# Kernel tuning notes

Hardware: AMD Instinct MI355X
Metric: run time of the kernel (lower is better)

## Reference

```python
import jax, jax.numpy as jnp
import numpy as np

B, M, K = 8, 4096, 16
C = 64       # input_dim
D = 64       # d_model


def _lin(key, fan_in, fan_out):
    k1, k2 = jax.random.split(key)
    bound = 1.0 / np.sqrt(fan_in)
    W = jax.random.uniform(k1, (fan_out, fan_in), minval=-bound, maxval=bound, dtype=jnp.float32)
    b = jax.random.uniform(k2, (fan_out,), minval=-bound, maxval=bound, dtype=jnp.float32)
    return W, b


def setup_inputs() -> dict:
    key = jax.random.key(0)
    ks = jax.random.split(key, 12)
    x = jax.random.normal(ks[0], (B, M, K, C), dtype=jnp.float32)
    xyz = jax.random.normal(ks[1], (B, M, K, 3), dtype=jnp.float32)
    Wq, bq = _lin(ks[2], C, D)
    Wk, bk = _lin(ks[3], C, D)
    Wv, bv = _lin(ks[4], C, D)
    Wp1, bp1 = _lin(ks[5], 3, D)
    Wp2, bp2 = _lin(ks[6], D, D)
    Wa1, ba1 = _lin(ks[7], D, D)
    Wa2, ba2 = _lin(ks[8], D, D)
    W2, b2 = _lin(ks[9], D, C)
    return dict(x=x, xyz=xyz, Wq=Wq, bq=bq, Wk=Wk, bk=bk, Wv=Wv, bv=bv,
                Wp1=Wp1, bp1=bp1, Wp2=Wp2, bp2=bp2,
                Wa1=Wa1, ba1=ba1, Wa2=Wa2, ba2=ba2, W2=W2, b2=b2)


def reference(x, xyz, Wq, bq, Wk, bk, Wv, bv, Wp1, bp1, Wp2, bp2,
              Wa1, ba1, Wa2, ba2, W2, b2):
    lin = lambda t, W, b: jnp.matmul(t, W.T) + b
    raw_feature = x[:, :, 0, :]                 # [B,M,C]
    raw_xyz = xyz[:, :, 0:1, :]                 # [B,M,1,3]
    q = lin(raw_feature, Wq, bq)                # [B,M,D]
    k = lin(x, Wk, bk)                          # [B,M,K,D]
    v = lin(x, Wv, bv)                          # [B,M,K,D]
    rel = xyz - raw_xyz                         # [B,M,K,3]
    pos_enc = lin(jax.nn.relu(lin(rel, Wp1, bp1)), Wp2, bp2)  # [B,M,K,D]
    h = q[:, :, None, :] - k + pos_enc          # [B,M,K,D]
    attn_logits = lin(jax.nn.relu(lin(h, Wa1, ba1)), Wa2, ba2)
    attn = jax.nn.softmax(attn_logits / np.sqrt(D), axis=-2)  # softmax over K
    res = jnp.einsum('bmnf,bmnf->bmf', attn, v + pos_enc)
    return lin(res, W2, b2) + raw_feature       # [B,M,C]
```

## Files before the change

kernel.cpp:

```cpp
#include <hip/hip_runtime.h>

#define NM 4096
#define NK 16
#define NC 64

typedef __attribute__((ext_vector_type(8))) short s8v;
typedef __attribute__((ext_vector_type(4))) float f4v;
typedef __attribute__((ext_vector_type(2))) unsigned int u2v;

__device__ __forceinline__ short f2bf(float f) {
  return __builtin_bit_cast(short, (__bf16)f);
}
__device__ __forceinline__ float bf2f(unsigned short s) {
  return __builtin_bit_cast(float, ((unsigned)s) << 16);
}
__device__ __forceinline__ s8v pack8(f4v a, f4v b) {
  s8v r;
  r[0]=f2bf(a[0]); r[1]=f2bf(a[1]); r[2]=f2bf(a[2]); r[3]=f2bf(a[3]);
  r[4]=f2bf(b[0]); r[5]=f2bf(b[1]); r[6]=f2bf(b[2]); r[7]=f2bf(b[3]);
  return r;
}

#define MFMA(a,b,c) __builtin_amdgcn_mfma_f32_16x16x32_bf16((a),(b),(c),0,0,0)

#define HSTRIDE 72
#define TB16 (16*HSTRIDE)

__global__ void precomp_kernel(const float* __restrict__ Wq, const float* __restrict__ bq,
                               const float* __restrict__ Wk, const float* __restrict__ bk,
                               const float* __restrict__ Wp2,const float* __restrict__ bp2,
                               const float* __restrict__ Wa1,const float* __restrict__ ba1,
                               float* __restrict__ ws) {
  const int gid = blockIdx.x * 256 + threadIdx.x;
  if (gid < 3*4096) {
    const int m = gid >> 12, e = gid & 4095, i = e >> 6, j = e & 63;
    const float* R = Wa1 + i*64;
    float s = 0.f;
    if (m == 0)      { for (int l = 0; l < 64; ++l) s += R[l] * Wq [l*64 + j]; }
    else if (m == 1) { for (int l = 0; l < 64; ++l) s -= R[l] * Wk [l*64 + j]; }
    else             { for (int l = 0; l < 64; ++l) s += R[l] * Wp2[l*64 + j]; }
    ws[gid] = s;
  } else if (gid < 3*4096 + 64) {
    const int i = gid - 3*4096;
    const float* R = Wa1 + i*64;
    float s = 0.f;
    for (int l = 0; l < 64; ++l) s += R[l] * bq[l];
    ws[gid] = s;
  } else if (gid < 3*4096 + 128) {
    const int i = gid - (3*4096 + 64);
    const float* R = Wa1 + i*64;
    float s = ba1[i];
    for (int l = 0; l < 64; ++l) s += R[l] * (bp2[l] - bk[l]);
    ws[gid] = s;
  }
}

__global__ void precomp2_kernel(const float* __restrict__ Wv,
                                const float* __restrict__ Wp2,
                                const float* __restrict__ Wa2,
                                const float* __restrict__ W2,
                                float* __restrict__ ws) {
  const int g = blockIdx.x * 256 + threadIdx.x;
  if (g >= 7*512) return;
  const int mat = g >> 9, rem = g & 511;
  const int f = rem >> 6, ln = rem & 63;
  const int t = f >> 1, h = f & 1;
  const int cc = ln & 15, qq = ln >> 4;
  const int n = 16*t + cc;
  const float* W =
    (mat==0) ? ws + 4096 :
    (mat==1) ? Wv :
    (mat==2) ? Wp2 :
    (mat==3) ? ws + 8192 :
    (mat==4) ? Wa2 :
    (mat==5) ? ws :
               W2;
  short* dst = (short*)(ws + 12544) + (size_t)g * 8;
  s8v v;
  #pragma unroll
  for (int j = 0; j < 8; ++j) {
    const int kp = h*32 + qq*8 + j;
    int k;
    if (mat == 4)                  k = 16*(2*h + (j>>2)) + 4*qq + (j&3);
    else if (mat == 2 || mat == 3) k = ((kp & 3) << 4) | (kp >> 2);
    else                           k = kp;
    v[j] = f2bf(W[n*64 + k]);
  }
  *(s8v*)dst = v;
}

__global__ __attribute__((amdgpu_flat_work_group_size(256, 256)))
           __attribute__((amdgpu_waves_per_eu(1, 8)))
void lattn_kernel(const float* __restrict__ x,  const float* __restrict__ xyz,
                  const float* __restrict__ Wp1,const float* __restrict__ bp1,
                  const float* __restrict__ Wp2,const float* __restrict__ bp2,
                  const float* __restrict__ Wv, const float* __restrict__ bv,
                  const float* __restrict__ Wa2,const float* __restrict__ ba2,
                  const float* __restrict__ W2, const float* __restrict__ b2,
                  const float* __restrict__ ws,
                  float* __restrict__ out) {
  __shared__ __align__(16) short wlds[5*8*64*8];
  __shared__ __align__(16) short qres[4*TB16];
  __shared__ __align__(16) f4v  wp1t[4*17];
  __shared__ float bvpet[64];
  __shared__ float ba2t[64];

  const int tid = threadIdx.x;
  const float* bqa = ws + 12288;
  const float* bcv = ws + 12352;
  const short* wsb = (const short*)(ws + 12544);

  #pragma unroll
  for (int i = 0; i < 10; ++i) {
    const int g = tid + i*256;
    *(s8v*)&wlds[(size_t)g*8] = *(const s8v*)&wsb[(size_t)g*8];
  }
  if (tid < 64) {
    const int lqv = tid >> 4, ii = tid & 15;
    const int jj = ii & 7, h = ii >> 3;
    const int n = 16*(jj&3) + 2*lqv + (jj>>2) + 8*h;
    f4v t4;
    t4[0] = Wp1[n*3+0]; t4[1] = Wp1[n*3+1]; t4[2] = Wp1[n*3+2]; t4[3] = bp1[n];
    wp1t[lqv*17 + ii] = t4;
  } else if (tid < 128) {
    const int n = tid - 64;
    bvpet[n] = bv[n] + bp2[n];
  } else if (tid < 192) {
    const int n = tid - 128;
    ba2t[n] = ba2[n];
  }
  __syncthreads();

  const int w    = tid >> 6;
  const int lane = tid & 63;
  const int c    = lane & 15;
  const int lq   = lane >> 4;

  const int gw  = blockIdx.x * 4 + w;
  const int gp0 = gw << 4;
  const int b   = gp0 >> 12;
  const int m0  = gp0 & (NM - 1);

  short* qbuf = qres + w * TB16;

  const long ptbase = (long)(b * NM + m0);

  {
    const float* xr = x + (ptbase + c) * (long)(NK*NC) + 8*lq;
    s8v rA0 = pack8(*(const f4v*)xr,        *(const f4v*)(xr+4));
    s8v rA1 = pack8(*(const f4v*)(xr+32),   *(const f4v*)(xr+36));
    #pragma unroll
    for (int t = 0; t < 4; ++t) {
      s8v w0 = *(const s8v*)&wsb[(size_t)(5*512 + 2*t*64 + lane)*8];
      s8v w1 = *(const s8v*)&wsb[(size_t)(5*512 + (2*t+1)*64 + lane)*8];
      const float bb = bqa[16*t + c];
      f4v acc = {bb, bb, bb, bb};
      acc = MFMA(rA0, w0, acc);
      acc = MFMA(rA1, w1, acc);
      const float bcf = bcv[16*t + c];
      #pragma unroll
      for (int r = 0; r < 4; ++r)
        qbuf[(4*lq + r)*HSTRIDE + 16*t + c] = f2bf(acc[r] + bcf);
    }
  }

  f4v na0, na1, na2, na3, nb0, nb1, nb2, nb3;
  float nzaa[3], nzba[3], nzab[3], nzbb[3];
  {
    const float* xra = x + ptbase * (long)(NK*NC) + c*NC + 8*lq;
    na0 = *(const f4v*)xra;      na1 = *(const f4v*)(xra+4);
    na2 = *(const f4v*)(xra+32); na3 = *(const f4v*)(xra+36);
    const float* xrb = xra + NK*NC;
    nb0 = *(const f4v*)xrb;      nb1 = *(const f4v*)(xrb+4);
    nb2 = *(const f4v*)(xrb+32); nb3 = *(const f4v*)(xrb+36);
    const float* zpa = xyz + ptbase * (long)(NK*3);
    nzaa[0]=zpa[c*3+0]; nzaa[1]=zpa[c*3+1]; nzaa[2]=zpa[c*3+2];
    nzba[0]=zpa[0];     nzba[1]=zpa[1];     nzba[2]=zpa[2];
    const float* zpb = zpa + NK*3;
    nzab[0]=zpb[c*3+0]; nzab[1]=zpb[c*3+1]; nzab[2]=zpb[c*3+2];
    nzbb[0]=zpb[0];     nzbb[1]=zpb[1];     nzbb[2]=zpb[2];
  }

  #pragma unroll 1
  for (int pp = 0; pp < 16; pp += 2) {
    s8v xAa0 = pack8(na0, na1), xAa1 = pack8(na2, na3);
    s8v xAb0 = pack8(nb0, nb1), xAb1 = pack8(nb2, nb3);
    const float rxa = nzaa[0]-nzba[0], rya = nzaa[1]-nzba[1], rza = nzaa[2]-nzba[2];
    const float rxb = nzab[0]-nzbb[0], ryb = nzab[1]-nzbb[1], rzb = nzab[2]-nzbb[2];
    if (pp < 14) {
      const long prow = ptbase + pp + 2;
      const float* xra = x + prow * (long)(NK*NC) + c*NC + 8*lq;
      na0 = *(const f4v*)xra;      na1 = *(const f4v*)(xra+4);
      na2 = *(const f4v*)(xra+32); na3 = *(const f4v*)(xra+36);
      const float* xrb = xra + NK*NC;
      nb0 = *(const f4v*)xrb;      nb1 = *(const f4v*)(xrb+4);
      nb2 = *(const f4v*)(xrb+32); nb3 = *(const f4v*)(xrb+36);
      const float* zpa = xyz + prow * (long)(NK*3);
      nzaa[0]=zpa[c*3+0]; nzaa[1]=zpa[c*3+1]; nzaa[2]=zpa[c*3+2];
      nzba[0]=zpa[0];     nzba[1]=zpa[1];     nzba[2]=zpa[2];
      const float* zpb = zpa + NK*3;
      nzab[0]=zpb[c*3+0]; nzab[1]=zpb[c*3+1]; nzab[2]=zpb[c*3+2];
      nzbb[0]=zpb[0];     nzbb[1]=zpb[1];     nzbb[2]=zpb[2];
    }

    s8v pAa0, pAa1, pAb0, pAb1;
    #pragma unroll
    for (int i = 0; i < 8; ++i) {
      f4v w0v = wp1t[lq*17 + i];
      f4v w1v = wp1t[lq*17 + 8 + i];
      float a0 = fmaxf(fmaf(w0v[0], rxa, fmaf(w0v[1], rya, fmaf(w0v[2], rza, w0v[3]))), 0.0f);
      float a1 = fmaxf(fmaf(w1v[0], rxa, fmaf(w1v[1], rya, fmaf(w1v[2], rza, w1v[3]))), 0.0f);
      float b0 = fmaxf(fmaf(w0v[0], rxb, fmaf(w0v[1], ryb, fmaf(w0v[2], rzb, w0v[3]))), 0.0f);
      float b1 = fmaxf(fmaf(w1v[0], rxb, fmaf(w1v[1], ryb, fmaf(w1v[2], rzb, w1v[3]))), 0.0f);
      pAa0[i] = f2bf(a0); pAa1[i] = f2bf(a1);
      pAb0[i] = f2bf(b0); pAb1[i] = f2bf(b1);
    }

    f4v sa[4], sb[4];
    #pragma unroll
    for (int t = 0; t < 4; ++t) {
      u2v qa2 = *(const u2v*)&qbuf[pp*HSTRIDE + 16*t + 4*lq];
      u2v qb2 = *(const u2v*)&qbuf[(pp+1)*HSTRIDE + 16*t + 4*lq];
      f4v acca, accb;
      acca[0] = __builtin_bit_cast(float, qa2[0] << 16);
      acca[1] = __builtin_bit_cast(float, qa2[0] & 0xffff0000u);
      acca[2] = __builtin_bit_cast(float, qa2[1] << 16);
      acca[3] = __builtin_bit_cast(float, qa2[1] & 0xffff0000u);
      accb[0] = __builtin_bit_cast(float, qb2[0] << 16);
      accb[1] = __builtin_bit_cast(float, qb2[0] & 0xffff0000u);
      accb[2] = __builtin_bit_cast(float, qb2[1] << 16);
      accb[3] = __builtin_bit_cast(float, qb2[1] & 0xffff0000u);
      const short* wb = &wlds[(0*512 + 2*t*64 + lane) * 8];
      s8v w0 = *(const s8v*)wb;
      s8v w1 = *(const s8v*)(wb + 512);
      acca = MFMA(w0, xAa0, acca);  acca = MFMA(w1, xAa1, acca);
      accb = MFMA(w0, xAb0, accb);  accb = MFMA(w1, xAb1, accb);
      sa[t] = acca; sb[t] = accb;
    }
    #pragma unroll
    for (int t = 0; t < 4; ++t) {
      const short* wb = &wlds[(3*512 + 2*t*64 + lane) * 8];
      s8v w0 = *(const s8v*)wb;
      s8v w1 = *(const s8v*)(wb + 512);
      f4v acca = MFMA(w0, pAa0, sa[t]);  acca = MFMA(w1, pAa1, acca);
      f4v accb = MFMA(w0, pAb0, sb[t]);  accb = MFMA(w1, pAb1, accb);
      #pragma unroll
      for (int r = 0; r < 4; ++r) {
        sa[t][r] = fmaxf(acca[r], 0.0f);
        sb[t][r] = fmaxf(accb[r], 0.0f);
      }
    }
    s8v aAa0 = pack8(sa[0], sa[1]), aAa1 = pack8(sa[2], sa[3]);
    s8v aAb0 = pack8(sb[0], sb[1]), aAb1 = pack8(sb[2], sb[3]);

    #pragma unroll
    for (int t = 0; t < 4; ++t) {
      const short* wb4 = &wlds[(4*512 + 2*t*64 + lane) * 8];
      s8v w40 = *(const s8v*)wb4;
      s8v w41 = *(const s8v*)(wb4 + 512);
      const float bb2 = ba2t[16*t + c];
      f4v lga = {bb2, bb2, bb2, bb2};
      f4v lgb = lga;
      lga = MFMA(aAa0, w40, lga);  lga = MFMA(aAa1, w41, lga);
      lgb = MFMA(aAb0, w40, lgb);  lgb = MFMA(aAb1, w41, lgb);

      const short* wb1 = &wlds[(1*512 + 2*t*64 + lane) * 8];
      const short* wb2 = &wlds[(2*512 + 2*t*64 + lane) * 8];
      s8v w10 = *(const s8v*)wb1;
      s8v w11 = *(const s8v*)(wb1 + 512);
      s8v w20 = *(const s8v*)wb2;
      s8v w21 = *(const s8v*)(wb2 + 512);
      const float bbv = bvpet[16*t + c];
      f4v vpa = {bbv, bbv, bbv, bbv};
      f4v vpb = vpa;
      vpa = MFMA(xAa0, w10, vpa);  vpa = MFMA(xAa1, w11, vpa);
      vpa = MFMA(pAa0, w20, vpa);  vpa = MFMA(pAa1, w21, vpa);
      vpb = MFMA(xAb0, w10, vpb);  vpb = MFMA(xAb1, w11, vpb);
      vpb = MFMA(pAb0, w20, vpb);  vpb = MFMA(pAb1, w21, vpb);

      f4v ea, eb;
      #pragma unroll
      for (int r = 0; r < 4; ++r) {
        ea[r] = exp2f(lga[r] * 0.18033688011112043f);
        eb[r] = exp2f(lgb[r] * 0.18033688011112043f);
      }
      float sma = (ea[0] + ea[1]) + (ea[2] + ea[3]);
      float smb = (eb[0] + eb[1]) + (eb[2] + eb[3]);
      sma += __shfl_xor(sma, 16);
      smb += __shfl_xor(smb, 16);
      sma += __shfl_xor(sma, 32);
      smb += __shfl_xor(smb, 32);
      float pra = 0.0f, prb = 0.0f;
      #pragma unroll
      for (int r = 0; r < 4; ++r) {
        pra += ea[r] * vpa[r];
        prb += eb[r] * vpb[r];
      }
      pra += __shfl_xor(pra, 16);
      prb += __shfl_xor(prb, 16);
      pra += __shfl_xor(pra, 32);
      prb += __shfl_xor(prb, 32);
      pra *= 1.0f / sma;
      prb *= 1.0f / smb;
      if (lq == 0) {
        qbuf[pp*HSTRIDE + 16*t + c]     = f2bf(pra);
        qbuf[(pp+1)*HSTRIDE + 16*t + c] = f2bf(prb);
      }
    }
  }

  {
    s8v resA0 = *(const s8v*)&qbuf[c*HSTRIDE + 8*lq];
    s8v resA1 = *(const s8v*)&qbuf[c*HSTRIDE + 32 + 8*lq];
    #pragma unroll
    for (int t = 0; t < 4; ++t) {
      s8v w0 = *(const s8v*)&wsb[(size_t)(6*512 + 2*t*64 + lane)*8];
      s8v w1 = *(const s8v*)&wsb[(size_t)(6*512 + (2*t+1)*64 + lane)*8];
      const float bb = b2[16*t + c];
      f4v acc = {bb, bb, bb, bb};
      acc = MFMA(resA0, w0, acc);
      acc = MFMA(resA1, w1, acc);
      #pragma unroll
      for (int r = 0; r < 4; ++r) {
        const long pr2 = ptbase + 4*lq + r;
        out[pr2*NC + 16*t + c] = acc[r] + x[pr2*(long)(NK*NC) + 16*t + c];
      }
    }
  }
}

extern "C" void kernel_launch(void* const* d_in, const int* in_sizes, int n_in,
                              void* d_out, int out_size, void* d_ws, size_t ws_size,
                              hipStream_t stream) {
  (void)in_sizes; (void)n_in; (void)out_size; (void)ws_size;
  const float* x   = (const float*)d_in[0];
  const float* xyz = (const float*)d_in[1];
  const float* Wq  = (const float*)d_in[2];
  const float* bq  = (const float*)d_in[3];
  const float* Wk  = (const float*)d_in[4];
  const float* bk  = (const float*)d_in[5];
  const float* Wv  = (const float*)d_in[6];
  const float* bv  = (const float*)d_in[7];
  const float* Wp1 = (const float*)d_in[8];
  const float* bp1 = (const float*)d_in[9];
  const float* Wp2 = (const float*)d_in[10];
  const float* bp2 = (const float*)d_in[11];
  const float* Wa1 = (const float*)d_in[12];
  const float* ba1 = (const float*)d_in[13];
  const float* Wa2 = (const float*)d_in[14];
  const float* ba2 = (const float*)d_in[15];
  const float* W2  = (const float*)d_in[16];
  const float* b2  = (const float*)d_in[17];
  float* out = (float*)d_out;
  float* ws  = (float*)d_ws;

  precomp_kernel<<<dim3(49), dim3(256), 0, stream>>>(Wq, bq, Wk, bk, Wp2, bp2, Wa1, ba1, ws);
  precomp2_kernel<<<dim3(14), dim3(256), 0, stream>>>(Wv, Wp2, Wa2, W2, ws);
  lattn_kernel<<<dim3(512), dim3(256), 0, stream>>>(
      x, xyz, Wp1, bp1, Wp2, bp2, Wv, bv, Wa2, ba2, W2, b2, ws, out);
}
```

Measured before the change: 244.5 us.

## Merge weight precompute kernels, hoist qbuf loads, add MFMA priority and fast math

Folds the two weight-preprocessing kernels into a single launch that computes the Wa1-composed products directly into the packed bf16 MFMA layout, removing one launch and the fp32 intermediate round trip. In the main kernel, the qbuf LDS reads are hoisted ahead of the position-MLP computation, s_setprio raises wave priority around the MFMA blocks, and exp2f and the reciprocal are swapped for the hardware intrinsics. Risks: each thread in the merged precompute now does redundant 64-length dot products serially, lowering its parallelism, and the fast exp and reciprocal are slightly less accurate.

```diff
diff --git a/kernel.cpp b/kernel.cpp
--- a/kernel.cpp
+++ b/kernel.cpp
@@ -10,9 +10,6 @@
 
 __device__ __forceinline__ short f2bf(float f) {
   return __builtin_bit_cast(short, (__bf16)f);
-}
-__device__ __forceinline__ float bf2f(unsigned short s) {
-  return __builtin_bit_cast(float, ((unsigned)s) << 16);
 }
 __device__ __forceinline__ s8v pack8(f4v a, f4v b) {
   s8v r;
@@ -30,63 +27,59 @@
                                const float* __restrict__ Wk, const float* __restrict__ bk,
                                const float* __restrict__ Wp2,const float* __restrict__ bp2,
                                const float* __restrict__ Wa1,const float* __restrict__ ba1,
+                               const float* __restrict__ Wv, const float* __restrict__ Wa2,
+                               const float* __restrict__ W2,
                                float* __restrict__ ws) {
   const int gid = blockIdx.x * 256 + threadIdx.x;
-  if (gid < 3*4096) {
-    const int m = gid >> 12, e = gid & 4095, i = e >> 6, j = e & 63;
-    const float* R = Wa1 + i*64;
-    float s = 0.f;
-    if (m == 0)      { for (int l = 0; l < 64; ++l) s += R[l] * Wq [l*64 + j]; }
-    else if (m == 1) { for (int l = 0; l < 64; ++l) s -= R[l] * Wk [l*64 + j]; }
-    else             { for (int l = 0; l < 64; ++l) s += R[l] * Wp2[l*64 + j]; }
-    ws[gid] = s;
-  } else if (gid < 3*4096 + 64) {
-    const int i = gid - 3*4096;
+  if (gid < 7*512) {
+    const int g = gid;
+    const int mat = g >> 9, rem = g & 511;
+    const int f = rem >> 6, ln = rem & 63;
+    const int t = f >> 1, h = f & 1;
+    const int cc = ln & 15, qq = ln >> 4;
+    const int n = 16*t + cc;
+    short* dst = (short*)(ws + 12544) + (size_t)g * 8;
+    s8v v;
+    #pragma unroll
+    for (int j = 0; j < 8; ++j) {
+      const int kp = h*32 + qq*8 + j;
+      int k;
+      if (mat == 4)                  k = 16*(2*h + (j>>2)) + 4*qq + (j&3);
+      else if (mat == 2 || mat == 3) k = ((kp & 3) << 4) | (kp >> 2);
+      else                           k = kp;
+      float val;
+      if (mat == 0) {
+        const float* R = Wa1 + n*64; float s = 0.f;
+        for (int l = 0; l < 64; ++l) s -= R[l] * Wk[l*64 + k];
+        val = s;
+      } else if (mat == 3) {
+        const float* R = Wa1 + n*64; float s = 0.f;
+        for (int l = 0; l < 64; ++l) s += R[l] * Wp2[l*64 + k];
+        val = s;
+      } else if (mat == 5) {
+        const float* R = Wa1 + n*64; float s = 0.f;
+        for (int l = 0; l < 64; ++l) s += R[l] * Wq[l*64 + k];
+        val = s;
+      } else {
+        const float* W = (mat==1) ? Wv : (mat==2) ? Wp2 : (mat==4) ? Wa2 : W2;
+        val = W[n*64 + k];
+      }
+      v[j] = f2bf(val);
+    }
+    *(s8v*)dst = v;
+  } else if (gid < 7*512 + 64) {
+    const int i = gid - 7*512;
     const float* R = Wa1 + i*64;
     float s = 0.f;
     for (int l = 0; l < 64; ++l) s += R[l] * bq[l];
-    ws[gid] = s;
-  } else if (gid < 3*4096 + 128) {
-    const int i = gid - (3*4096 + 64);
+    ws[12288 + i] = s;
+  } else if (gid < 7*512 + 128) {
+    const int i = gid - (7*512 + 64);
     const float* R = Wa1 + i*64;
     float s = ba1[i];
     for (int l = 0; l < 64; ++l) s += R[l] * (bp2[l] - bk[l]);
-    ws[gid] = s;
-  }
-}
-
-__global__ void precomp2_kernel(const float* __restrict__ Wv,
-                                const float* __restrict__ Wp2,
-                                const float* __restrict__ Wa2,
-                                const float* __restrict__ W2,
-                                float* __restrict__ ws) {
-  const int g = blockIdx.x * 256 + threadIdx.x;
-  if (g >= 7*512) return;
-  const int mat = g >> 9, rem = g & 511;
-  const int f = rem >> 6, ln = rem & 63;
-  const int t = f >> 1, h = f & 1;
-  const int cc = ln & 15, qq = ln >> 4;
-  const int n = 16*t + cc;
-  const float* W =
-    (mat==0) ? ws + 4096 :
-    (mat==1) ? Wv :
-    (mat==2) ? Wp2 :
-    (mat==3) ? ws + 8192 :
-    (mat==4) ? Wa2 :
-    (mat==5) ? ws :
-               W2;
-  short* dst = (short*)(ws + 12544) + (size_t)g * 8;
-  s8v v;
-  #pragma unroll
-  for (int j = 0; j < 8; ++j) {
-    const int kp = h*32 + qq*8 + j;
-    int k;
-    if (mat == 4)                  k = 16*(2*h + (j>>2)) + 4*qq + (j&3);
-    else if (mat == 2 || mat == 3) k = ((kp & 3) << 4) | (kp >> 2);
-    else                           k = kp;
-    v[j] = f2bf(W[n*64 + k]);
-  }
-  *(s8v*)dst = v;
+    ws[12352 + i] = s;
+  }
 }
 
 __global__ __attribute__((amdgpu_flat_work_group_size(256, 256)))
@@ -203,6 +196,15 @@
       nzbb[0]=zpb[0];     nzbb[1]=zpb[1];     nzbb[2]=zpb[2];
     }
 
+    u2v qa2_0 = *(const u2v*)&qbuf[pp*HSTRIDE +  0 + 4*lq];
+    u2v qa2_1 = *(const u2v*)&qbuf[pp*HSTRIDE + 16 + 4*lq];
+    u2v qa2_2 = *(const u2v*)&qbuf[pp*HSTRIDE + 32 + 4*lq];
+    u2v qa2_3 = *(const u2v*)&qbuf[pp*HSTRIDE + 48 + 4*lq];
+    u2v qb2_0 = *(const u2v*)&qbuf[(pp+1)*HSTRIDE +  0 + 4*lq];
+    u2v qb2_1 = *(const u2v*)&qbuf[(pp+1)*HSTRIDE + 16 + 4*lq];
+    u2v qb2_2 = *(const u2v*)&qbuf[(pp+1)*HSTRIDE + 32 + 4*lq];
+    u2v qb2_3 = *(const u2v*)&qbuf[(pp+1)*HSTRIDE + 48 + 4*lq];
+
     s8v pAa0, pAa1, pAb0, pAb1;
     #pragma unroll
     for (int i = 0; i < 8; ++i) {
@@ -217,10 +219,11 @@
     }
 
     f4v sa[4], sb[4];
-    #pragma unroll
-    for (int t = 0; t < 4; ++t) {
-      u2v qa2 = *(const u2v*)&qbuf[pp*HSTRIDE + 16*t + 4*lq];
-      u2v qb2 = *(const u2v*)&qbuf[(pp+1)*HSTRIDE + 16*t + 4*lq];
+    __builtin_amdgcn_s_setprio(1);
+    #pragma unroll
+    for (int t = 0; t < 4; ++t) {
+      u2v qa2 = (t==0) ? qa2_0 : (t==1) ? qa2_1 : (t==2) ? qa2_2 : qa2_3;
+      u2v qb2 = (t==0) ? qb2_0 : (t==1) ? qb2_1 : (t==2) ? qb2_2 : qb2_3;
       f4v acca, accb;
       acca[0] = __builtin_bit_cast(float, qa2[0] << 16);
       acca[1] = __builtin_bit_cast(float, qa2[0] & 0xffff0000u);
@@ -250,6 +253,7 @@
         sb[t][r] = fmaxf(accb[r], 0.0f);
       }
     }
+    __builtin_amdgcn_s_setprio(0);
     s8v aAa0 = pack8(sa[0], sa[1]), aAa1 = pack8(sa[2], sa[3]);
     s8v aAb0 = pack8(sb[0], sb[1]), aAb1 = pack8(sb[2], sb[3]);
 
@@ -259,6 +263,7 @@
       s8v w40 = *(const s8v*)wb4;
       s8v w41 = *(const s8v*)(wb4 + 512);
       const float bb2 = ba2t[16*t + c];
+      __builtin_amdgcn_s_setprio(1);
       f4v lga = {bb2, bb2, bb2, bb2};
       f4v lgb = lga;
       lga = MFMA(aAa0, w40, lga);  lga = MFMA(aAa1, w41, lga);
@@ -277,12 +282,13 @@
       vpa = MFMA(pAa0, w20, vpa);  vpa = MFMA(pAa1, w21, vpa);
       vpb = MFMA(xAb0, w10, vpb);  vpb = MFMA(xAb1, w11, vpb);
       vpb = MFMA(pAb0, w20, vpb);  vpb = MFMA(pAb1, w21, vpb);
+      __builtin_amdgcn_s_setprio(0);
 
       f4v ea, eb;
       #pragma unroll
       for (int r = 0; r < 4; ++r) {
-        ea[r] = exp2f(lga[r] * 0.18033688011112043f);
-        eb[r] = exp2f(lgb[r] * 0.18033688011112043f);
+        ea[r] = __builtin_amdgcn_exp2f(lga[r] * 0.18033688011112043f);
+        eb[r] = __builtin_amdgcn_exp2f(lgb[r] * 0.18033688011112043f);
       }
       float sma = (ea[0] + ea[1]) + (ea[2] + ea[3]);
       float smb = (eb[0] + eb[1]) + (eb[2] + eb[3]);
@@ -300,8 +306,8 @@
       prb += __shfl_xor(prb, 16);
       pra += __shfl_xor(pra, 32);
       prb += __shfl_xor(prb, 32);
-      pra *= 1.0f / sma;
-      prb *= 1.0f / smb;
+      pra *= __builtin_amdgcn_rcpf(sma);
+      prb *= __builtin_amdgcn_rcpf(smb);
       if (lq == 0) {
         qbuf[pp*HSTRIDE + 16*t + c]     = f2bf(pra);
         qbuf[(pp+1)*HSTRIDE + 16*t + c] = f2bf(prb);
@@ -354,8 +360,8 @@
   float* out = (float*)d_out;
   float* ws  = (float*)d_ws;
 
-  precomp_kernel<<<dim3(49), dim3(256), 0, stream>>>(Wq, bq, Wk, bk, Wp2, bp2, Wa1, ba1, ws);
-  precomp2_kernel<<<dim3(14), dim3(256), 0, stream>>>(Wv, Wp2, Wa2, W2, ws);
+  precomp_kernel<<<dim3(15), dim3(256), 0, stream>>>(
+      Wq, bq, Wk, bk, Wp2, bp2, Wa1, ba1, Wv, Wa2, W2, ws);
   lattn_kernel<<<dim3(512), dim3(256), 0, stream>>>(
       x, xyz, Wp1, bp1, Wp2, bp2, Wv, bv, Wa2, ba2, W2, b2, ws, out);
 }
```

Result: slower. 257.1 us (+5.2%).
